# Kernel tuning notes

Hardware: AMD Instinct MI355X
Metric: run time of the kernel (lower is better)

Reference implementation:

```python
import jax, jax.numpy as jnp
import numpy as np

D_MODEL = 1024
N_HEADS = 16
D_K = D_MODEL // N_HEADS
LORA_R = 8
SCALING = 16 / 8  # lora_alpha / lora_rank = 2.0


def setup_inputs() -> dict:
    key = jax.random.key(0)
    ks = jax.random.split(key, 12)
    s = 1.0 / np.sqrt(D_MODEL)
    inp = {
        "x": jax.random.normal(ks[0], (4, 2048, D_MODEL), dtype=jnp.float32),
        "w_q": jax.random.normal(ks[1], (D_MODEL, D_MODEL), dtype=jnp.float32) * s,
        "b_q": jnp.zeros((D_MODEL,), dtype=jnp.float32),
        "w_k": jax.random.normal(ks[2], (D_MODEL, D_MODEL), dtype=jnp.float32) * s,
        "b_k": jnp.zeros((D_MODEL,), dtype=jnp.float32),
        "w_v": jax.random.normal(ks[3], (D_MODEL, D_MODEL), dtype=jnp.float32) * s,
        "b_v": jnp.zeros((D_MODEL,), dtype=jnp.float32),
        "w_o": jax.random.normal(ks[4], (D_MODEL, D_MODEL), dtype=jnp.float32) * s,
        "b_o": jnp.zeros((D_MODEL,), dtype=jnp.float32),
        # LoRA: down [d_model -> r], up [r -> d_model]; up init nonzero here so grads flow
        "a_q": jax.random.normal(ks[5], (D_MODEL, LORA_R), dtype=jnp.float32) * s,
        "u_q": jax.random.normal(ks[6], (LORA_R, D_MODEL), dtype=jnp.float32) * 0.01,
        "a_k": jax.random.normal(ks[7], (D_MODEL, LORA_R), dtype=jnp.float32) * s,
        "u_k": jax.random.normal(ks[8], (LORA_R, D_MODEL), dtype=jnp.float32) * 0.01,
        "a_v": jax.random.normal(ks[9], (D_MODEL, LORA_R), dtype=jnp.float32) * s,
        "u_v": jax.random.normal(ks[10], (LORA_R, D_MODEL), dtype=jnp.float32) * 0.01,
    }
    return inp


def reference(x, w_q, b_q, w_k, b_k, w_v, b_v, w_o, b_o, a_q, u_q, a_k, u_k, a_v, u_v):
    B, S, D = x.shape
    # base projections + LoRA (eval mode: dropout off)
    q = x @ w_q + b_q + (x @ a_q) @ u_q * SCALING
    k = x @ w_k + b_k + (x @ a_k) @ u_k * SCALING
    v = x @ w_v + b_v + (x @ a_v) @ u_v * SCALING
    # [B, H, S, d_k]
    q = q.reshape(B, S, N_HEADS, D_K).transpose(0, 2, 1, 3)
    k = k.reshape(B, S, N_HEADS, D_K).transpose(0, 2, 1, 3)
    v = v.reshape(B, S, N_HEADS, D_K).transpose(0, 2, 1, 3)
    scores = jnp.einsum("bhsd,bhtd->bhst", q, k) / np.sqrt(D_K)
    probs = jax.nn.softmax(scores, axis=-1)
    out = jnp.einsum("bhst,bhtd->bhsd", probs, v)
    out = out.transpose(0, 2, 1, 3).reshape(B, S, D)
    return out @ w_o + b_o
```

## Files before the change

kernel.cpp:

```cpp
#include <hip/hip_runtime.h>
#include <stdint.h>

typedef unsigned short u16;
typedef unsigned int u32;
typedef __bf16 bf16x8 __attribute__((ext_vector_type(8)));
typedef __bf16 bf16x4 __attribute__((ext_vector_type(4)));
typedef float f32x4 __attribute__((ext_vector_type(4)));

#define SEQ 2048
#define QSCALE 0.1803368801111137f

__device__ __forceinline__ float fast_exp2(float x) {
#if __has_builtin(__builtin_amdgcn_exp2f)
  return __builtin_amdgcn_exp2f(x);
#else
  return exp2f(x);
#endif
}

__device__ __forceinline__ void async16(const void* g, void* l) {
  __builtin_amdgcn_global_load_lds((const __attribute__((address_space(1))) void*)g,
                                   (__attribute__((address_space(3))) void*)l, 16, 0, 0);
}


__global__ void conv_x_kernel(const float* __restrict__ x, u16* __restrict__ xb) {
  int i = (blockIdx.x * 256 + threadIdx.x) * 4;
  float4 v = *(const float4*)(x + i);
  bf16x4 o;
  o[0] = (__bf16)v.x; o[1] = (__bf16)v.y; o[2] = (__bf16)v.z; o[3] = (__bf16)v.w;
  *(bf16x4*)(xb + i) = o;
}

__global__ void prep_w_kernel(const float* __restrict__ wq, const float* __restrict__ wk,
                              const float* __restrict__ wv, const float* __restrict__ wo,
                              const float* __restrict__ aq, const float* __restrict__ ak,
                              const float* __restrict__ av,
                              const float* __restrict__ uq, const float* __restrict__ uk,
                              const float* __restrict__ uv,
                              u16* __restrict__ weffT) {
  const int p = blockIdx.y;
  const int tn0 = (blockIdx.x & 31) * 32, tk0 = (blockIdx.x >> 5) * 32;
  const float* w = (p == 0) ? wq : (p == 1) ? wk : (p == 2) ? wv : wo;
  const float* a = (p == 0) ? aq : (p == 1) ? ak : av;
  const float* u = (p == 0) ? uq : (p == 1) ? uk : uv;
  __shared__ float wt[32][33];
  __shared__ float at[32][8];
  __shared__ float ut[8][33];
  const int t = threadIdx.x;
  {
    int tk = t >> 3, tn4 = (t & 7) * 4;
    float4 v = *(const float4*)(w + (tk0 + tk) * 1024 + tn0 + tn4);
    wt[tk][tn4] = v.x; wt[tk][tn4 + 1] = v.y; wt[tk][tn4 + 2] = v.z; wt[tk][tn4 + 3] = v.w;
  }
  if (p < 3) {
    at[t >> 3][t & 7] = a[(tk0 + (t >> 3)) * 8 + (t & 7)];
    ut[t >> 5][t & 31] = u[(t >> 5) * 1024 + tn0 + (t & 31)];
  }
  __syncthreads();
  const int tn = t >> 3, tk4 = (t & 7) * 4;
  bf16x4 o;
#pragma unroll
  for (int jj = 0; jj < 4; ++jj) {
    int k = tk4 + jj;
    float val = wt[k][tn];
    if (p < 3) {
      float acc = 0.f;
#pragma unroll
      for (int r = 0; r < 8; ++r) acc += at[k][r] * ut[r][tn];
      val += 2.0f * acc;
    }
    if (p == 0) val *= QSCALE;
    o[jj] = (__bf16)val;
  }
  *(bf16x4*)(weffT + p * 1048576 + (tn0 + tn) * 1024 + tk0 + tk4) = o;
}

__global__ void prep_bias_kernel(const float* __restrict__ bq, const float* __restrict__ bk,
                                 const float* __restrict__ bv, float* __restrict__ bias_qkv) {
  int i = blockIdx.x * 256 + threadIdx.x;
  bias_qkv[i] = (i < 1024) ? bq[i] * QSCALE : (i < 2048) ? bk[i - 1024] : bv[i - 2048];
}


template <int MODE>
__global__ __launch_bounds__(256, 2)
void gemm_tt(const u16* __restrict__ U, const u16* __restrict__ V, void* __restrict__ OUT,
             u16* __restrict__ vT, const float* __restrict__ bias, const int NU, const int K) {
  __shared__ __align__(16) char smU[8192];
  __shared__ __align__(16) char smV[8192];
  const int t = threadIdx.x;
  const int lane = t & 63, ln = lane & 15, g = lane >> 4, w = t >> 6;
  const int u0 = blockIdx.x * 128, v0 = blockIdx.y * 128;
  const int wu = (w & 1) * 64, wv = (w >> 1) * 64;
  f32x4 acc[4][4] = {};
  for (int k0 = 0; k0 < K; k0 += 32) {
    __syncthreads();
#pragma unroll
    for (int half = 0; half < 2; ++half) {
      int p = half * 256 + t;
      int s = p >> 2, cp = p & 3;
      int c = cp ^ (s & 3);
      int ldsoff = (half * 256 + (t & 192)) * 16;
      async16(U + (u0 + s) * K + k0 + c * 8, smU + ldsoff);
      async16(V + (v0 + s) * K + k0 + c * 8, smV + ldsoff);
    }
    __syncthreads();
    bf16x8 af[4], bf[4];
#pragma unroll
    for (int mt = 0; mt < 4; ++mt)
      af[mt] = *(const bf16x8*)(smU + (wu + mt * 16 + ln) * 64 + ((g ^ (ln & 3)) * 16));
#pragma unroll
    for (int nt = 0; nt < 4; ++nt)
      bf[nt] = *(const bf16x8*)(smV + (wv + nt * 16 + ln) * 64 + ((g ^ (ln & 3)) * 16));
#pragma unroll
    for (int mt = 0; mt < 4; ++mt)
#pragma unroll
      for (int nt = 0; nt < 4; ++nt)
        acc[mt][nt] = __builtin_amdgcn_mfma_f32_16x16x32_bf16(af[mt], bf[nt], acc[mt][nt], 0, 0, 0);
  }
  const bool isV = (MODE == 1) && (u0 + wu >= 2048);
#pragma unroll
  for (int mt = 0; mt < 4; ++mt) {
    const int u = u0 + wu + mt * 16 + g * 4;
    const float4 bs = *(const float4*)(bias + u);
#pragma unroll
    for (int nt = 0; nt < 4; ++nt) {
      const int v = v0 + wv + nt * 16 + ln;
      f32x4 a = acc[mt][nt];
      a[0] += bs.x; a[1] += bs.y; a[2] += bs.z; a[3] += bs.w;
      if (MODE == 0) {
        *(float4*)((float*)OUT + (size_t)v * NU + u) = make_float4(a[0], a[1], a[2], a[3]);
      } else if (!isV) {
        bf16x4 o;
        o[0] = (__bf16)a[0]; o[1] = (__bf16)a[1]; o[2] = (__bf16)a[2]; o[3] = (__bf16)a[3];
        *(bf16x4*)((u16*)OUT + (size_t)v * 2048 + u) = o;
      } else {
        const int uu = u - 2048;
        const int hh = uu >> 6, dd = uu & 63;
        const int bb = v >> 11, ss = v & 2047;
        u16* dst = vT + ((size_t)((bb * 16 + hh) * 64 + dd)) * 2048 + ss;
#pragma unroll
        for (int r = 0; r < 4; ++r)
          *(__bf16*)(dst + (size_t)r * 2048) = (__bf16)a[r];
      }
    }
  }
}


__global__ __launch_bounds__(256, 2)
void attn_kernel(const u16* __restrict__ qkv, const u16* __restrict__ vT,
                 u16* __restrict__ attn_o) {
  __shared__ __align__(16) char smK[16384];
  __shared__ __align__(16) char smVt[20480];
  __shared__ __align__(16) char smP[8192];
  const int t = threadIdx.x;
  const int lane = t & 63, ln = lane & 15, g = lane >> 4, w = t >> 6;
  const int h = blockIdx.x, qt = blockIdx.y, b = blockIdx.z;
  const int q0 = qt * 128;
  const size_t base_b = (size_t)b * SEQ * 2048;
  const u16* qbase = qkv + base_b + h * 64;
  const u16* kbase0 = qkv + base_b + 1024 + h * 64;
  const u16* vbase0 = vT + ((size_t)(b * 16 + h) * 64) * 2048;

  {
    u32 val = ((t >> 4) == 0) ? 0x3F803F80u : 0u;
    uint4 q4 = {val, val, val, val};
    *(uint4*)(smVt + 16384 + t * 16) = q4;
  }

  bf16x8 qf[2][2];
#pragma unroll
  for (int kk = 0; kk < 2; ++kk)
#pragma unroll
    for (int nt = 0; nt < 2; ++nt)
      qf[kk][nt] = *(const bf16x8*)(qbase + (size_t)(q0 + w * 32 + nt * 16 + ln) * 2048 +
                                    kk * 32 + g * 8);

  const u16* srcK[4];
  const u16* srcV[4];
  char* dstK[4];
  char* dstV[4];
#pragma unroll
  for (int i = 0; i < 4; ++i) {
    int p = i * 256 + t;
    {
      int row = p >> 3, cp = p & 7, c = cp ^ (row & 7);
      srcK[i] = kbase0 + (size_t)row * 2048 + c * 8;
      dstK[i] = smK + (i * 256 + (t & 192)) * 16;
    }
    {
      int d = p >> 4, cp = p & 15;
      int key = (d & 15) ^ (d >> 3);
      int c = (cp ^ key) & 15;
      srcV[i] = vbase0 + (size_t)d * 2048 + c * 8;
      dstV[i] = smVt + (i * 256 + (t & 192)) * 16;
    }
  }

  f32x4 accO[5][2] = {};

  for (int kt = 0; kt < 16; ++kt) {
    __syncthreads();
#pragma unroll
    for (int i = 0; i < 4; ++i) {
      async16(srcK[i], dstK[i]);
      srcK[i] += 128 * 2048;
    }
#pragma unroll
    for (int i = 0; i < 4; ++i) {
      async16(srcV[i], dstV[i]);
      srcV[i] += 128;
    }
    __syncthreads();
    f32x4 st[8][2] = {};
#pragma unroll
    for (int kk = 0; kk < 2; ++kk) {
#pragma unroll
      for (int mt = 0; mt < 8; ++mt) {
        int row = mt * 16 + ln;
        bf16x8 kf = *(const bf16x8*)(smK + row * 128 + (((4 * kk + g) ^ (ln & 7)) * 16));
        st[mt][0] = __builtin_amdgcn_mfma_f32_16x16x32_bf16(kf, qf[kk][0], st[mt][0], 0, 0, 0);
        st[mt][1] = __builtin_amdgcn_mfma_f32_16x16x32_bf16(kf, qf[kk][1], st[mt][1], 0, 0, 0);
      }
    }
    char* pw = smP + w * 2048;
#pragma unroll
    for (int kk = 0; kk < 4; ++kk) {
#pragma unroll
      for (int mt2 = 0; mt2 < 2; ++mt2)
#pragma unroll
        for (int nt = 0; nt < 2; ++nt) {
          f32x4 sv = st[kk * 2 + mt2][nt];
          bf16x4 pk;
#pragma unroll
          for (int r = 0; r < 4; ++r) pk[r] = (__bf16)fast_exp2(sv[r]);
          int q = nt * 16 + ln;
          int c = 2 * mt2 + (g >> 1);
          *(bf16x4*)(pw + q * 64 + (((c ^ ((q >> 2) & 3)) & 3) * 16) + (g & 1) * 8) = pk;
        }
      int keyr = (ln >> 2) & 3;
      bf16x8 pf0 = *(const bf16x8*)(pw + ln * 64 + (((g ^ keyr) & 3) * 16));
      bf16x8 pf1 = *(const bf16x8*)(pw + (16 + ln) * 64 + (((g ^ keyr) & 3) * 16));
#pragma unroll
      for (int ot = 0; ot < 5; ++ot) {
        int row = ot * 16 + ln;
        int key = (row & 15) ^ (row >> 3);
        bf16x8 vf = *(const bf16x8*)(smVt + row * 256 + (((4 * kk + g) ^ key) & 15) * 16);
        accO[ot][0] = __builtin_amdgcn_mfma_f32_16x16x32_bf16(vf, pf0, accO[ot][0], 0, 0, 0);
        accO[ot][1] = __builtin_amdgcn_mfma_f32_16x16x32_bf16(vf, pf1, accO[ot][1], 0, 0, 0);
      }
    }
  }
#pragma unroll
  for (int nt = 0; nt < 2; ++nt) {
    float lv = __shfl(accO[4][nt][0], ln);
    float il = 1.0f / lv;
    const int s = q0 + w * 32 + nt * 16 + ln;
#pragma unroll
    for (int ot = 0; ot < 4; ++ot) {
      bf16x4 o;
#pragma unroll
      for (int r = 0; r < 4; ++r) o[r] = (__bf16)(accO[ot][nt][r] * il);
      *(bf16x4*)(attn_o + (size_t)(b * SEQ + s) * 1024 + h * 64 + ot * 16 + g * 4) = o;
    }
  }
}


extern "C" void kernel_launch(void* const* d_in, const int* in_sizes, int n_in,
                              void* d_out, int out_size, void* d_ws, size_t ws_size,
                              hipStream_t stream) {
  const float* x  = (const float*)d_in[0];
  const float* wq = (const float*)d_in[1];
  const float* bq = (const float*)d_in[2];
  const float* wk = (const float*)d_in[3];
  const float* bk = (const float*)d_in[4];
  const float* wv = (const float*)d_in[5];
  const float* bv = (const float*)d_in[6];
  const float* wo = (const float*)d_in[7];
  const float* bo = (const float*)d_in[8];
  const float* aq = (const float*)d_in[9];
  const float* uq = (const float*)d_in[10];
  const float* ak = (const float*)d_in[11];
  const float* uk = (const float*)d_in[12];
  const float* av = (const float*)d_in[13];
  const float* uv = (const float*)d_in[14];

  char* ws = (char*)d_ws;
  u16* xb       = (u16*)(ws);
  u16* attn_o   = (u16*)(ws);
  u16* qkv      = (u16*)(ws + (16u << 20));
  u16* vT       = (u16*)(ws + (48u << 20));
  u16* weffT    = (u16*)(ws + (64u << 20));
  float* biasq  = (float*)(ws + (72u << 20));

  conv_x_kernel<<<dim3(8192), dim3(256), 0, stream>>>(x, xb);
  prep_w_kernel<<<dim3(1024, 4), dim3(256), 0, stream>>>(wq, wk, wv, wo, aq, ak, av, uq, uk, uv, weffT);
  prep_bias_kernel<<<dim3(12), dim3(256), 0, stream>>>(bq, bk, bv, biasq);
  gemm_tt<1><<<dim3(24, 64), dim3(256), 0, stream>>>(weffT, xb, (void*)qkv, vT, biasq, 2048, 1024);
  attn_kernel<<<dim3(16, 16, 4), dim3(256), 0, stream>>>(qkv, vT, attn_o);
  gemm_tt<0><<<dim3(8, 64), dim3(256), 0, stream>>>(weffT + 3u * 1048576u, attn_o, d_out, nullptr, bo, 1024, 1024);
}
```

Baseline: 301.9 us.

## Use 32x32 MFMA in attention with register-shuffled P and merge prep kernels

The attention kernel moves from 16x16x32 to 32x32x16 bf16 MFMA. The exponentiated score tile is repacked into the PV operand layout using cross-half lane shuffles instead of a round trip through shared memory. The row sum is now accumulated in registers rather than through an extra ones-row in V, which frees the smP buffer and the padded V buffer, and launch bounds are raised to 3 blocks per CU. The three prep kernels (x conversion, weight fold, bias) are merged into one launch to cut launch overhead. Risks include higher register pressure from 16-wide accumulators and the extra shuffle cost.

```diff
diff --git a/kernel.cpp b/kernel.cpp
--- a/kernel.cpp
+++ b/kernel.cpp
@@ -6,80 +6,83 @@
 typedef __bf16 bf16x8 __attribute__((ext_vector_type(8)));
 typedef __bf16 bf16x4 __attribute__((ext_vector_type(4)));
 typedef float f32x4 __attribute__((ext_vector_type(4)));
+typedef float f32x16 __attribute__((ext_vector_type(16)));
+typedef u32 u32x4 __attribute__((ext_vector_type(4)));
 
 #define SEQ 2048
 #define QSCALE 0.1803368801111137f
 
-__device__ __forceinline__ float fast_exp2(float x) {
-#if __has_builtin(__builtin_amdgcn_exp2f)
-  return __builtin_amdgcn_exp2f(x);
-#else
-  return exp2f(x);
-#endif
-}
+__device__ __forceinline__ float fast_exp2(float x) { return __builtin_amdgcn_exp2f(x); }
 
 __device__ __forceinline__ void async16(const void* g, void* l) {
   __builtin_amdgcn_global_load_lds((const __attribute__((address_space(1))) void*)g,
                                    (__attribute__((address_space(3))) void*)l, 16, 0, 0);
 }
 
-
-__global__ void conv_x_kernel(const float* __restrict__ x, u16* __restrict__ xb) {
-  int i = (blockIdx.x * 256 + threadIdx.x) * 4;
-  float4 v = *(const float4*)(x + i);
-  bf16x4 o;
-  o[0] = (__bf16)v.x; o[1] = (__bf16)v.y; o[2] = (__bf16)v.z; o[3] = (__bf16)v.w;
-  *(bf16x4*)(xb + i) = o;
-}
-
-__global__ void prep_w_kernel(const float* __restrict__ wq, const float* __restrict__ wk,
-                              const float* __restrict__ wv, const float* __restrict__ wo,
-                              const float* __restrict__ aq, const float* __restrict__ ak,
-                              const float* __restrict__ av,
-                              const float* __restrict__ uq, const float* __restrict__ uk,
-                              const float* __restrict__ uv,
-                              u16* __restrict__ weffT) {
-  const int p = blockIdx.y;
-  const int tn0 = (blockIdx.x & 31) * 32, tk0 = (blockIdx.x >> 5) * 32;
-  const float* w = (p == 0) ? wq : (p == 1) ? wk : (p == 2) ? wv : wo;
-  const float* a = (p == 0) ? aq : (p == 1) ? ak : av;
-  const float* u = (p == 0) ? uq : (p == 1) ? uk : uv;
+__device__ __forceinline__ u32 pkbf(float a, float b) {
+  u16 xa = __builtin_bit_cast(u16, (__bf16)a);
+  u16 xb = __builtin_bit_cast(u16, (__bf16)b);
+  return (u32)xa | ((u32)xb << 16);
+}
+
+
+__global__ void prep_all_kernel(const float* __restrict__ x, u16* __restrict__ xb,
+                                const float* __restrict__ wq, const float* __restrict__ wk,
+                                const float* __restrict__ wv, const float* __restrict__ wo,
+                                const float* __restrict__ aq, const float* __restrict__ ak,
+                                const float* __restrict__ av,
+                                const float* __restrict__ uq, const float* __restrict__ uk,
+                                const float* __restrict__ uv,
+                                u16* __restrict__ weffT,
+                                const float* __restrict__ bq, const float* __restrict__ bk,
+                                const float* __restrict__ bv, float* __restrict__ bias_qkv) {
   __shared__ float wt[32][33];
   __shared__ float at[32][8];
   __shared__ float ut[8][33];
+  const int bid = blockIdx.x;
   const int t = threadIdx.x;
-  {
-    int tk = t >> 3, tn4 = (t & 7) * 4;
-    float4 v = *(const float4*)(w + (tk0 + tk) * 1024 + tn0 + tn4);
-    wt[tk][tn4] = v.x; wt[tk][tn4 + 1] = v.y; wt[tk][tn4 + 2] = v.z; wt[tk][tn4 + 3] = v.w;
-  }
-  if (p < 3) {
-    at[t >> 3][t & 7] = a[(tk0 + (t >> 3)) * 8 + (t & 7)];
-    ut[t >> 5][t & 31] = u[(t >> 5) * 1024 + tn0 + (t & 31)];
-  }
-  __syncthreads();
-  const int tn = t >> 3, tk4 = (t & 7) * 4;
-  bf16x4 o;
-#pragma unroll
-  for (int jj = 0; jj < 4; ++jj) {
-    int k = tk4 + jj;
-    float val = wt[k][tn];
+  if (bid < 8192) {
+    int i = (bid * 256 + t) * 4;
+    float4 v = *(const float4*)(x + i);
+    bf16x4 o;
+    o[0] = (__bf16)v.x; o[1] = (__bf16)v.y; o[2] = (__bf16)v.z; o[3] = (__bf16)v.w;
+    *(bf16x4*)(xb + i) = o;
+  } else if (bid < 12288) {
+    const int p = (bid - 8192) >> 10, bx = (bid - 8192) & 1023;
+    const int tn0 = (bx & 31) * 32, tk0 = (bx >> 5) * 32;
+    const float* w = (p == 0) ? wq : (p == 1) ? wk : (p == 2) ? wv : wo;
+    const float* a = (p == 0) ? aq : (p == 1) ? ak : av;
+    const float* u = (p == 0) ? uq : (p == 1) ? uk : uv;
+    {
+      int tk = t >> 3, tn4 = (t & 7) * 4;
+      float4 v = *(const float4*)(w + (tk0 + tk) * 1024 + tn0 + tn4);
+      wt[tk][tn4] = v.x; wt[tk][tn4 + 1] = v.y; wt[tk][tn4 + 2] = v.z; wt[tk][tn4 + 3] = v.w;
+    }
     if (p < 3) {
-      float acc = 0.f;
-#pragma unroll
-      for (int r = 0; r < 8; ++r) acc += at[k][r] * ut[r][tn];
-      val += 2.0f * acc;
-    }
-    if (p == 0) val *= QSCALE;
-    o[jj] = (__bf16)val;
-  }
-  *(bf16x4*)(weffT + p * 1048576 + (tn0 + tn) * 1024 + tk0 + tk4) = o;
-}
-
-__global__ void prep_bias_kernel(const float* __restrict__ bq, const float* __restrict__ bk,
-                                 const float* __restrict__ bv, float* __restrict__ bias_qkv) {
-  int i = blockIdx.x * 256 + threadIdx.x;
-  bias_qkv[i] = (i < 1024) ? bq[i] * QSCALE : (i < 2048) ? bk[i - 1024] : bv[i - 2048];
+      at[t >> 3][t & 7] = a[(tk0 + (t >> 3)) * 8 + (t & 7)];
+      ut[t >> 5][t & 31] = u[(t >> 5) * 1024 + tn0 + (t & 31)];
+    }
+    __syncthreads();
+    const int tn = t >> 3, tk4 = (t & 7) * 4;
+    bf16x4 o;
+#pragma unroll
+    for (int jj = 0; jj < 4; ++jj) {
+      int k = tk4 + jj;
+      float val = wt[k][tn];
+      if (p < 3) {
+        float acc = 0.f;
+#pragma unroll
+        for (int r = 0; r < 8; ++r) acc += at[k][r] * ut[r][tn];
+        val += 2.0f * acc;
+      }
+      if (p == 0) val *= QSCALE;
+      o[jj] = (__bf16)val;
+    }
+    *(bf16x4*)(weffT + p * 1048576 + (tn0 + tn) * 1024 + tk0 + tk4) = o;
+  } else {
+    int i = (bid - 12288) * 256 + t;
+    bias_qkv[i] = (i < 1024) ? bq[i] * QSCALE : (i < 2048) ? bk[i - 1024] : bv[i - 2048];
+  }
 }
 
 
@@ -149,34 +152,24 @@
 }
 
 
-__global__ __launch_bounds__(256, 2)
+__global__ __launch_bounds__(256, 3)
 void attn_kernel(const u16* __restrict__ qkv, const u16* __restrict__ vT,
                  u16* __restrict__ attn_o) {
   __shared__ __align__(16) char smK[16384];
-  __shared__ __align__(16) char smVt[20480];
-  __shared__ __align__(16) char smP[8192];
+  __shared__ __align__(16) char smVt[16384];
   const int t = threadIdx.x;
-  const int lane = t & 63, ln = lane & 15, g = lane >> 4, w = t >> 6;
-  const int h = blockIdx.x, qt = blockIdx.y, b = blockIdx.z;
+  const int lane = t & 63, q32 = lane & 31, hf = lane >> 5, w = t >> 6;
+  const int hd = blockIdx.x, qt = blockIdx.y, b = blockIdx.z;
   const int q0 = qt * 128;
   const size_t base_b = (size_t)b * SEQ * 2048;
-  const u16* qbase = qkv + base_b + h * 64;
-  const u16* kbase0 = qkv + base_b + 1024 + h * 64;
-  const u16* vbase0 = vT + ((size_t)(b * 16 + h) * 64) * 2048;
-
-  {
-    u32 val = ((t >> 4) == 0) ? 0x3F803F80u : 0u;
-    uint4 q4 = {val, val, val, val};
-    *(uint4*)(smVt + 16384 + t * 16) = q4;
-  }
-
-  bf16x8 qf[2][2];
-#pragma unroll
-  for (int kk = 0; kk < 2; ++kk)
-#pragma unroll
-    for (int nt = 0; nt < 2; ++nt)
-      qf[kk][nt] = *(const bf16x8*)(qbase + (size_t)(q0 + w * 32 + nt * 16 + ln) * 2048 +
-                                    kk * 32 + g * 8);
+  const u16* qbase = qkv + base_b + hd * 64;
+  const u16* kbase0 = qkv + base_b + 1024 + hd * 64;
+  const u16* vbase0 = vT + ((size_t)(b * 16 + hd) * 64) * 2048;
+
+  bf16x8 qf[4];
+#pragma unroll
+  for (int ks = 0; ks < 4; ++ks)
+    qf[ks] = *(const bf16x8*)(qbase + (size_t)(q0 + w * 32 + q32) * 2048 + ks * 16 + hf * 8);
 
   const u16* srcK[4];
   const u16* srcV[4];
@@ -199,7 +192,8 @@
     }
   }
 
-  f32x4 accO[5][2] = {};
+  f32x16 accO[2] = {};
+  float l_acc = 0.f;
 
   for (int kt = 0; kt < 16; ++kt) {
     __syncthreads();
@@ -214,58 +208,67 @@
       srcV[i] += 128;
     }
     __syncthreads();
-    f32x4 st[8][2] = {};
-#pragma unroll
-    for (int kk = 0; kk < 2; ++kk) {
-#pragma unroll
-      for (int mt = 0; mt < 8; ++mt) {
-        int row = mt * 16 + ln;
-        bf16x8 kf = *(const bf16x8*)(smK + row * 128 + (((4 * kk + g) ^ (ln & 7)) * 16));
-        st[mt][0] = __builtin_amdgcn_mfma_f32_16x16x32_bf16(kf, qf[kk][0], st[mt][0], 0, 0, 0);
-        st[mt][1] = __builtin_amdgcn_mfma_f32_16x16x32_bf16(kf, qf[kk][1], st[mt][1], 0, 0, 0);
-      }
-    }
-    char* pw = smP + w * 2048;
-#pragma unroll
-    for (int kk = 0; kk < 4; ++kk) {
-#pragma unroll
-      for (int mt2 = 0; mt2 < 2; ++mt2)
-#pragma unroll
-        for (int nt = 0; nt < 2; ++nt) {
-          f32x4 sv = st[kk * 2 + mt2][nt];
-          bf16x4 pk;
-#pragma unroll
-          for (int r = 0; r < 4; ++r) pk[r] = (__bf16)fast_exp2(sv[r]);
-          int q = nt * 16 + ln;
-          int c = 2 * mt2 + (g >> 1);
-          *(bf16x4*)(pw + q * 64 + (((c ^ ((q >> 2) & 3)) & 3) * 16) + (g & 1) * 8) = pk;
+
+    f32x16 st[4] = {};
+#pragma unroll
+    for (int ks = 0; ks < 4; ++ks) {
+#pragma unroll
+      for (int c = 0; c < 4; ++c) {
+        int row = c * 32 + q32;
+        bf16x8 kfr = *(const bf16x8*)(smK + row * 128 + (((2 * ks + hf) ^ (row & 7)) * 16));
+        st[c] = __builtin_amdgcn_mfma_f32_32x32x16_bf16(kfr, qf[ks], st[c], 0, 0, 0);
+      }
+    }
+
+#pragma unroll
+    for (int c = 0; c < 4; ++c) {
+      float e[16];
+#pragma unroll
+      for (int r = 0; r < 16; ++r) {
+        e[r] = fast_exp2(st[c][r]);
+        l_acc += e[r];
+      }
+#pragma unroll
+      for (int kh = 0; kh < 2; ++kh) {
+        u32 A0 = pkbf(e[8 * kh + 0], e[8 * kh + 1]);
+        u32 A1 = pkbf(e[8 * kh + 2], e[8 * kh + 3]);
+        u32 A2 = pkbf(e[8 * kh + 4], e[8 * kh + 5]);
+        u32 A3 = pkbf(e[8 * kh + 6], e[8 * kh + 7]);
+        u32 t0 = hf ? A0 : A2;
+        u32 t1 = hf ? A1 : A3;
+        u32 P0 = (u32)__shfl_xor((int)t0, 32);
+        u32 P1 = (u32)__shfl_xor((int)t1, 32);
+        u32x4 bw;
+        bw[0] = hf ? P0 : A0;
+        bw[1] = hf ? P1 : A1;
+        bw[2] = hf ? A2 : P0;
+        bw[3] = hf ? A3 : P1;
+        bf16x8 pfrag = __builtin_bit_cast(bf16x8, bw);
+#pragma unroll
+        for (int mt = 0; mt < 2; ++mt) {
+          int row = mt * 32 + q32;
+          int key = (row & 15) ^ (row >> 3);
+          bf16x8 vfr = *(const bf16x8*)(smVt + row * 256 +
+                                        (((4 * c + 2 * kh + hf) ^ key) & 15) * 16);
+          accO[mt] = __builtin_amdgcn_mfma_f32_32x32x16_bf16(vfr, pfrag, accO[mt], 0, 0, 0);
         }
-      int keyr = (ln >> 2) & 3;
-      bf16x8 pf0 = *(const bf16x8*)(pw + ln * 64 + (((g ^ keyr) & 3) * 16));
-      bf16x8 pf1 = *(const bf16x8*)(pw + (16 + ln) * 64 + (((g ^ keyr) & 3) * 16));
-#pragma unroll
-      for (int ot = 0; ot < 5; ++ot) {
-        int row = ot * 16 + ln;
-        int key = (row & 15) ^ (row >> 3);
-        bf16x8 vf = *(const bf16x8*)(smVt + row * 256 + (((4 * kk + g) ^ key) & 15) * 16);
-        accO[ot][0] = __builtin_amdgcn_mfma_f32_16x16x32_bf16(vf, pf0, accO[ot][0], 0, 0, 0);
-        accO[ot][1] = __builtin_amdgcn_mfma_f32_16x16x32_bf16(vf, pf1, accO[ot][1], 0, 0, 0);
-      }
-    }
-  }
-#pragma unroll
-  for (int nt = 0; nt < 2; ++nt) {
-    float lv = __shfl(accO[4][nt][0], ln);
-    float il = 1.0f / lv;
-    const int s = q0 + w * 32 + nt * 16 + ln;
-#pragma unroll
-    for (int ot = 0; ot < 4; ++ot) {
+      }
+    }
+  }
+
+  float l_tot = l_acc + __shfl_xor(l_acc, 32);
+  float il = 1.0f / l_tot;
+  const int s = q0 + w * 32 + q32;
+#pragma unroll
+  for (int mt = 0; mt < 2; ++mt)
+#pragma unroll
+    for (int qd = 0; qd < 4; ++qd) {
+      int d0 = 32 * mt + 8 * qd + 4 * hf;
       bf16x4 o;
 #pragma unroll
-      for (int r = 0; r < 4; ++r) o[r] = (__bf16)(accO[ot][nt][r] * il);
-      *(bf16x4*)(attn_o + (size_t)(b * SEQ + s) * 1024 + h * 64 + ot * 16 + g * 4) = o;
-    }
-  }
+      for (int r = 0; r < 4; ++r) o[r] = (__bf16)(accO[mt][4 * qd + r] * il);
+      *(bf16x4*)(attn_o + (size_t)(b * SEQ + s) * 1024 + hd * 64 + d0) = o;
+    }
 }
 
 
@@ -296,9 +299,8 @@
   u16* weffT    = (u16*)(ws + (64u << 20));
   float* biasq  = (float*)(ws + (72u << 20));
 
-  conv_x_kernel<<<dim3(8192), dim3(256), 0, stream>>>(x, xb);
-  prep_w_kernel<<<dim3(1024, 4), dim3(256), 0, stream>>>(wq, wk, wv, wo, aq, ak, av, uq, uk, uv, weffT);
-  prep_bias_kernel<<<dim3(12), dim3(256), 0, stream>>>(bq, bk, bv, biasq);
+  prep_all_kernel<<<dim3(12300), dim3(256), 0, stream>>>(
+      x, xb, wq, wk, wv, wo, aq, ak, av, uq, uk, uv, weffT, bq, bk, bv, biasq);
   gemm_tt<1><<<dim3(24, 64), dim3(256), 0, stream>>>(weffT, xb, (void*)qkv, vT, biasq, 2048, 1024);
   attn_kernel<<<dim3(16, 16, 4), dim3(256), 0, stream>>>(qkv, vT, attn_o);
   gemm_tt<0><<<dim3(8, 64), dim3(256), 0, stream>>>(weffT + 3u * 1048576u, attn_o, d_out, nullptr, bo, 1024, 1024);
```

After: 313.1 us. +3.7%, slower.
